# Performance work log

Measured on AMD Instinct MI355X. Metric: run time of the kernel, lower is better.

The kernel has to match this reference:

```python
import jax, jax.numpy as jnp
import numpy as np

M1, M2 = 32, 32  # max_modes1, max_modes2
C_IN, C_OUT = 64, 64


def _neg_k(a):
    # torch.roll(torch.flip(a, dims=[-2,-1]), shifts=(1,1), dims=[-2,-1])
    return jnp.roll(jnp.flip(a, axis=(-2, -1)), shift=(1, 1), axis=(-2, -1))


def compl_mul2d(x1, x2):
    x1n = _neg_k(x1)
    x2n = _neg_k(x2)
    e = lambda a, b: jnp.einsum('bixy,ioxy->boxy', a, b)
    return 0.5 * (e(x1, x2) - e(x1n, x2n) + e(x1, x2n) + e(x1n, x2))


def setup_inputs() -> dict:
    key = jax.random.key(0)
    k1, k2, k3 = jax.random.split(key, 3)
    scale = 1.0 / (C_IN * C_OUT)
    return {
        "x": jax.random.normal(k1, (16, C_IN, 256, 256), dtype=jnp.float32),
        "weights1_re": scale * jax.random.uniform(k2, (C_IN, C_OUT, M1, M2), dtype=jnp.float32),
        "weights1_im": scale * jax.random.uniform(k3, (C_IN, C_OUT, M1, M2), dtype=jnp.float32),
        "error_estimate": 1,  # must be >= 1: smaller modes would break the einsum vs full weights
    }


def reference(x, weights1_re, weights1_im, error_estimate):
    B, Ci, H, W = x.shape
    modes1 = min(M1, max(1, int(M1 * error_estimate)))
    modes2 = min(M2, max(1, int(M2 * error_estimate)))
    weights1 = jax.lax.complex(weights1_re, weights1_im)  # complex64

    # spectral branch (computed exactly as in the original; note the original
    # module never uses out_ft in its return value)
    x_ft = jnp.fft.rfftn(x, axes=(2, 3))  # [B, Ci, H, W//2+1] complex64
    block = compl_mul2d(x_ft[:, :, :modes1, :modes2], weights1)
    out_ft = jnp.zeros((B, C_OUT, H, W // 2 + 1), dtype=jnp.complex64)
    out_ft = out_ft.at[:, :, :modes1, :modes2].set(block)

    # idht(x) with dim=None: fftn over ALL axes, (real+imag)/numel
    X = jnp.fft.fftn(x, axes=(0, 1, 2, 3))
    out = (X.real + X.imag) / x.size
    return out.astype(jnp.float32)
```

## Files before the change

kernel.cpp:

```cpp
#include <hip/hip_runtime.h>


#define NB 16
#define NC 64
#define NH 256
#define NW 256
#define WP 132
#define CSTRIDE (NH*WP)
#define BSTRIDE (NC*NH*WP)
#define LSTRIDE (NH*WP)

__device__ __forceinline__ float2 cadd(float2 a, float2 b){ return make_float2(a.x+b.x, a.y+b.y); }
__device__ __forceinline__ float2 csub(float2 a, float2 b){ return make_float2(a.x-b.x, a.y-b.y); }
__device__ __forceinline__ float2 cmul(float2 a, float2 b){ return make_float2(a.x*b.x - a.y*b.y, a.x*b.y + a.y*b.x); }

__device__ __forceinline__ float2 twd(float frac){
  float sn, cs;
  __sincosf(-6.28318530717958647692f * frac, &sn, &cs);
  return make_float2(cs, sn);
}

__device__ __forceinline__ void dft4(float2&a,float2&b,float2&c,float2&d){
  float2 t0=cadd(a,c), t1=csub(a,c), t2=cadd(b,d), t3=csub(b,d);
  float2 t3i = make_float2(t3.y, -t3.x);
  a=cadd(t0,t2); c=csub(t0,t2); b=cadd(t1,t3i); d=csub(t1,t3i);
}

__device__ __forceinline__ void fft8(float2 v[8]){
  float2 e0=v[0],e1=v[2],e2=v[4],e3=v[6];
  float2 o0=v[1],o1=v[3],o2=v[5],o3=v[7];
  dft4(e0,e1,e2,e3); dft4(o0,o1,o2,o3);
  const float s=0.70710678118654752440f;
  float2 w1o=make_float2(s*(o1.x+o1.y), s*(o1.y-o1.x));
  float2 w2o=make_float2(o2.y, -o2.x);
  float2 w3o=make_float2(s*(o3.y-o3.x), -s*(o3.x+o3.y));
  v[0]=cadd(e0,o0); v[4]=csub(e0,o0);
  v[1]=cadd(e1,w1o); v[5]=csub(e1,w1o);
  v[2]=cadd(e2,w2o); v[6]=csub(e2,w2o);
  v[3]=cadd(e3,w3o); v[7]=csub(e3,w3o);
}

__device__ __forceinline__ void fft16(float2 v[16]){
  float2 e[8], o[8];
#pragma unroll
  for(int i=0;i<8;i++){ e[i]=v[2*i]; o[i]=v[2*i+1]; }
  fft8(e); fft8(o);
  const float c1=0.92387953251128675613f, s1=0.38268343236508977173f, s=0.70710678118654752440f;
  const float wr[8] = {1.f,  c1,  s,  s1, 0.f, -s1, -s, -c1};
  const float wi[8] = {0.f, -s1, -s, -c1, -1.f, -c1, -s, -s1};
#pragma unroll
  for(int k=0;k<8;k++){
    float2 wo = make_float2(wr[k]*o[k].x - wi[k]*o[k].y, wr[k]*o[k].y + wi[k]*o[k].x);
    v[k]=cadd(e[k],wo); v[k+8]=csub(e[k],wo);
  }
}

__global__ __launch_bounds__(256) void k1_fftW(const float* __restrict__ x, float2* __restrict__ S){
  __shared__ float2 lds[16][16][17];
  const int j    = threadIdx.x & 15;
  const int line = threadIdx.x >> 4;
  const int gline = blockIdx.x * 16 + line;
  const float* px = x + (size_t)gline * NW;
  float2 v[16];
#pragma unroll
  for(int n1=0;n1<16;n1++) v[n1] = make_float2(px[16*n1 + j], 0.f);
  fft16(v);
#pragma unroll
  for(int k1=0;k1<16;k1++){
    v[k1] = cmul(v[k1], twd((float)(j*k1) * (1.0f/256.0f)));
    lds[line][k1][j] = v[k1];
  }
  __syncthreads();
  float2 u[16];
#pragma unroll
  for(int n2=0;n2<16;n2++) u[n2] = lds[line][j][n2];
  fft16(u);
  float2* ps = S + (size_t)gline * WP;
#pragma unroll
  for(int k2=0;k2<8;k2++) ps[j + 16*k2] = u[k2];
  if(j==0) ps[128] = u[8];
}

__global__ __launch_bounds__(256) void k2_fftH(float2* __restrict__ S){
  __shared__ float2 lds[16][16][17];
  const int kwo  = threadIdx.x & 15;
  const int j    = threadIdx.x >> 4;
  const int tile = blockIdx.x % 9;
  const int slice= blockIdx.x / 9;
  const int kw   = tile*16 + kwo;
  const bool act = (kw <= 128);
  float2* base = S + (size_t)slice * NH * WP + kw;
  float2 v[16];
#pragma unroll
  for(int n1=0;n1<16;n1++) v[n1] = act ? base[(16*n1 + j) * WP] : make_float2(0.f,0.f);
  fft16(v);
#pragma unroll
  for(int k1=0;k1<16;k1++){
    v[k1] = cmul(v[k1], twd((float)(j*k1) * (1.0f/256.0f)));
    lds[kwo][k1][j] = v[k1];
  }
  __syncthreads();
  float2 u[16];
#pragma unroll
  for(int n2=0;n2<16;n2++) u[n2] = lds[kwo][j][n2];
  fft16(u);
  if(act){
#pragma unroll
    for(int k2=0;k2<16;k2++) base[(j + 16*k2) * WP] = u[k2];
  }
}

__global__ __launch_bounds__(256) void k3_fused(const float2* __restrict__ S, float* __restrict__ out){
  __shared__ float2 A[1024][9];
  const int t    = threadIdx.x;
  const int h    = blockIdx.x & 255;
  const int tile = blockIdx.x >> 8;
  const int kw0  = tile * 8;
  const float2* Sbase = S + (size_t)h * WP + kw0;

#pragma unroll
  for(int r=0;r<16;r++){
    int f    = t + 256*r;
    int line = f >> 2;
    int part = f & 3;
    float4 val;
    if(kw0 + part*2 + 1 < WP){
      val = *(const float4*)(Sbase + (size_t)line * LSTRIDE + part*2);
    } else {
      val = make_float4(0.f,0.f,0.f,0.f);
    }
    A[line][part*2]     = make_float2(val.x, val.y);
    A[line][part*2 + 1] = make_float2(val.z, val.w);
  }
  __syncthreads();

#pragma unroll
  for(int q=0;q<4;q++){
    int item = t + 256*q;
    int kwo = item & 7, n2 = (item>>3) & 7, b = item >> 6;
    float2 v[8];
#pragma unroll
    for(int n1=0;n1<8;n1++) v[n1] = A[b*64 + 8*n1 + n2][kwo];
    fft8(v);
#pragma unroll
    for(int k1=0;k1<8;k1++) A[b*64 + 8*k1 + n2][kwo] = cmul(v[k1], twd((float)(n2*k1) * (1.0f/64.0f)));
  }
  __syncthreads();

  {
    float2 u[4][8];
#pragma unroll
    for(int q=0;q<4;q++){
      int item = t + 256*q;
      int kwo = item & 7, k1 = (item>>3) & 7, b = item >> 6;
#pragma unroll
      for(int n2=0;n2<8;n2++) u[q][n2] = A[b*64 + 8*k1 + n2][kwo];
      fft8(u[q]);
    }
    __syncthreads();
#pragma unroll
    for(int q=0;q<4;q++){
      int item = t + 256*q;
      int kwo = item & 7, k1 = (item>>3) & 7, b = item >> 6;
#pragma unroll
      for(int k2=0;k2<8;k2++) A[b*64 + (k1 + 8*k2)][kwo] = u[q][k2];
    }
  }
  __syncthreads();

  const float inv = 1.0f / 67108864.0f;
  const int h2 = (NH - h) & 255;
#pragma unroll
  for(int q=0;q<2;q++){
    int item = t + 256*q;
    int kwo = item & 7, kc = item >> 3;
    float2 v[16];
#pragma unroll
    for(int b=0;b<16;b++) v[b] = A[b*64 + kc][kwo];
    fft16(v);
    const int kw = kw0 + kwo;
    if(kw <= 128){
      const int kc2 = (NC - kc) & 63;
#pragma unroll
      for(int kb=0;kb<16;kb++){
        float2 z = v[kb];
        out[(((size_t)kb*NC + kc)*NH + h)*NW + kw] = (z.x + z.y) * inv;
        if(kw >= 1 && kw <= 127){
          const int kb2 = (16 - kb) & 15;
          out[(((size_t)kb2*NC + kc2)*NH + h2)*NW + (NW - kw)] = (z.x - z.y) * inv;
        }
      }
    }
  }
}

extern "C" void kernel_launch(void* const* d_in, const int* in_sizes, int n_in,
                              void* d_out, int out_size, void* d_ws, size_t ws_size,
                              hipStream_t stream) {
  const float* x = (const float*)d_in[0];
  float* out = (float*)d_out;
  float2* S  = (float2*)d_ws;

  k1_fftW<<<NB*NC*NH/16, 256, 0, stream>>>(x, S);
  k2_fftH<<<NB*NC*9,     256, 0, stream>>>(S);
  k3_fused<<<17*256,     256, 0, stream>>>(S, out);
}
```

Measured before the change: 908.3 us.

## Stage k1 input via float4 LDS loads and widen k3 tiles with swizzled LDS

k1 now loads each block's 16 input rows into shared memory with coalesced float4 reads before the radix-16 passes, instead of strided scalar global reads. k3 processes 16 frequency columns per block with 1024 threads and stores its tile in an XOR-swizzled shared-memory layout, cutting the block count from 17*256 to 9*256 and making the staging stores 16-byte wide. The intent is better global coalescing and fewer LDS bank conflicts. The cost is 128 KB of LDS per k3 block, which limits occupancy to about one block per CU, plus an extra barrier in k1.

```diff
diff --git a/kernel.cpp b/kernel.cpp
--- a/kernel.cpp
+++ b/kernel.cpp
@@ -6,8 +6,6 @@
 #define NH 256
 #define NW 256
 #define WP 132
-#define CSTRIDE (NH*WP)
-#define BSTRIDE (NC*NH*WP)
 #define LSTRIDE (NH*WP)
 
 __device__ __forceinline__ float2 cadd(float2 a, float2 b){ return make_float2(a.x+b.x, a.y+b.y); }
@@ -56,33 +54,47 @@
 }
 
 __global__ __launch_bounds__(256) void k1_fftW(const float* __restrict__ x, float2* __restrict__ S){
-  __shared__ float2 lds[16][16][17];
-  const int j    = threadIdx.x & 15;
-  const int line = threadIdx.x >> 4;
-  const int gline = blockIdx.x * 16 + line;
-  const float* px = x + (size_t)gline * NW;
+  __shared__ __align__(16) float smem[16*273*2];
+  float2* lds2 = (float2*)smem;
+  const int t    = threadIdx.x;
+  const int j    = t & 15;
+  const int line = t >> 4;
+  const size_t gbase = (size_t)blockIdx.x * 16;
+
+  const float4* xv = (const float4*)x;
+#pragma unroll
+  for(int r=0;r<4;r++){
+    int f  = r*256 + t;
+    int ln = f >> 6, pos = f & 63;
+    float4 val = xv[(gbase + ln) * 64 + pos];
+    *(float4*)(&smem[ln*264 + pos*4]) = val;
+  }
+  __syncthreads();
+
   float2 v[16];
 #pragma unroll
-  for(int n1=0;n1<16;n1++) v[n1] = make_float2(px[16*n1 + j], 0.f);
+  for(int n1=0;n1<16;n1++) v[n1] = make_float2(smem[line*264 + 16*n1 + j], 0.f);
+  __syncthreads();
+
   fft16(v);
 #pragma unroll
   for(int k1=0;k1<16;k1++){
     v[k1] = cmul(v[k1], twd((float)(j*k1) * (1.0f/256.0f)));
-    lds[line][k1][j] = v[k1];
+    lds2[line*273 + k1*17 + j] = v[k1];
   }
   __syncthreads();
   float2 u[16];
 #pragma unroll
-  for(int n2=0;n2<16;n2++) u[n2] = lds[line][j][n2];
+  for(int n2=0;n2<16;n2++) u[n2] = lds2[line*273 + j*17 + n2];
   fft16(u);
-  float2* ps = S + (size_t)gline * WP;
+  float2* ps = S + (gbase + line) * WP;
 #pragma unroll
   for(int k2=0;k2<8;k2++) ps[j + 16*k2] = u[k2];
   if(j==0) ps[128] = u[8];
 }
 
 __global__ __launch_bounds__(256) void k2_fftH(float2* __restrict__ S){
-  __shared__ float2 lds[16][16][17];
+  __shared__ float2 lds[16*273];
   const int kwo  = threadIdx.x & 15;
   const int j    = threadIdx.x >> 4;
   const int tile = blockIdx.x % 9;
@@ -97,12 +109,12 @@
 #pragma unroll
   for(int k1=0;k1<16;k1++){
     v[k1] = cmul(v[k1], twd((float)(j*k1) * (1.0f/256.0f)));
-    lds[kwo][k1][j] = v[k1];
+    lds[kwo*273 + k1*17 + j] = v[k1];
   }
   __syncthreads();
   float2 u[16];
 #pragma unroll
-  for(int n2=0;n2<16;n2++) u[n2] = lds[kwo][j][n2];
+  for(int n2=0;n2<16;n2++) u[n2] = lds[kwo*273 + j*17 + n2];
   fft16(u);
   if(act){
 #pragma unroll
@@ -110,73 +122,71 @@
   }
 }
 
-__global__ __launch_bounds__(256) void k3_fused(const float2* __restrict__ S, float* __restrict__ out){
-  __shared__ float2 A[1024][9];
+#define AIX(row,kwo) (((row)<<4) + ((kwo) ^ (((row)&7)<<1)))
+__global__ __launch_bounds__(1024) void k3_fused(const float2* __restrict__ S, float* __restrict__ out){
+  __shared__ __align__(16) float2 A[1024*16];
   const int t    = threadIdx.x;
   const int h    = blockIdx.x & 255;
   const int tile = blockIdx.x >> 8;
-  const int kw0  = tile * 8;
+  const int kw0  = tile * 16;
   const float2* Sbase = S + (size_t)h * WP + kw0;
 
 #pragma unroll
-  for(int r=0;r<16;r++){
-    int f    = t + 256*r;
-    int line = f >> 2;
-    int part = f & 3;
+  for(int r=0;r<8;r++){
+    int f    = t + 1024*r;
+    int line = f >> 3;
+    int part = f & 7;
     float4 val;
     if(kw0 + part*2 + 1 < WP){
       val = *(const float4*)(Sbase + (size_t)line * LSTRIDE + part*2);
     } else {
       val = make_float4(0.f,0.f,0.f,0.f);
     }
-    A[line][part*2]     = make_float2(val.x, val.y);
-    A[line][part*2 + 1] = make_float2(val.z, val.w);
-  }
-  __syncthreads();
-
-#pragma unroll
-  for(int q=0;q<4;q++){
-    int item = t + 256*q;
-    int kwo = item & 7, n2 = (item>>3) & 7, b = item >> 6;
+    *(float4*)(&A[AIX(line, part*2)]) = val;
+  }
+  __syncthreads();
+
+#pragma unroll
+  for(int q=0;q<2;q++){
+    int item = t + 1024*q;
+    int kwo = item & 15, n2 = (item>>4) & 7, b = item >> 7;
     float2 v[8];
 #pragma unroll
-    for(int n1=0;n1<8;n1++) v[n1] = A[b*64 + 8*n1 + n2][kwo];
+    for(int n1=0;n1<8;n1++) v[n1] = A[AIX(b*64 + 8*n1 + n2, kwo)];
     fft8(v);
 #pragma unroll
-    for(int k1=0;k1<8;k1++) A[b*64 + 8*k1 + n2][kwo] = cmul(v[k1], twd((float)(n2*k1) * (1.0f/64.0f)));
+    for(int k1=0;k1<8;k1++) A[AIX(b*64 + 8*k1 + n2, kwo)] = cmul(v[k1], twd((float)(n2*k1) * (1.0f/64.0f)));
   }
   __syncthreads();
 
   {
-    float2 u[4][8];
-#pragma unroll
-    for(int q=0;q<4;q++){
-      int item = t + 256*q;
-      int kwo = item & 7, k1 = (item>>3) & 7, b = item >> 6;
-#pragma unroll
-      for(int n2=0;n2<8;n2++) u[q][n2] = A[b*64 + 8*k1 + n2][kwo];
+    float2 u[2][8];
+#pragma unroll
+    for(int q=0;q<2;q++){
+      int item = t + 1024*q;
+      int kwo = item & 15, k1 = (item>>4) & 7, b = item >> 7;
+#pragma unroll
+      for(int n2=0;n2<8;n2++) u[q][n2] = A[AIX(b*64 + 8*k1 + n2, kwo)];
       fft8(u[q]);
     }
     __syncthreads();
 #pragma unroll
-    for(int q=0;q<4;q++){
-      int item = t + 256*q;
-      int kwo = item & 7, k1 = (item>>3) & 7, b = item >> 6;
-#pragma unroll
-      for(int k2=0;k2<8;k2++) A[b*64 + (k1 + 8*k2)][kwo] = u[q][k2];
+    for(int q=0;q<2;q++){
+      int item = t + 1024*q;
+      int kwo = item & 15, k1 = (item>>4) & 7, b = item >> 7;
+#pragma unroll
+      for(int k2=0;k2<8;k2++) A[AIX(b*64 + (k1 + 8*k2), kwo)] = u[q][k2];
     }
   }
   __syncthreads();
 
   const float inv = 1.0f / 67108864.0f;
   const int h2 = (NH - h) & 255;
-#pragma unroll
-  for(int q=0;q<2;q++){
-    int item = t + 256*q;
-    int kwo = item & 7, kc = item >> 3;
+  {
+    int kwo = t & 15, kc = t >> 4;
     float2 v[16];
 #pragma unroll
-    for(int b=0;b<16;b++) v[b] = A[b*64 + kc][kwo];
+    for(int b=0;b<16;b++) v[b] = A[AIX(b*64 + kc, kwo)];
     fft16(v);
     const int kw = kw0 + kwo;
     if(kw <= 128){
@@ -201,7 +211,7 @@
   float* out = (float*)d_out;
   float2* S  = (float2*)d_ws;
 
-  k1_fftW<<<NB*NC*NH/16, 256, 0, stream>>>(x, S);
-  k2_fftH<<<NB*NC*9,     256, 0, stream>>>(S);
-  k3_fused<<<17*256,     256, 0, stream>>>(S, out);
-}
+  k1_fftW<<<NB*NC*NH/16, 256,  0, stream>>>(x, S);
+  k2_fftH<<<NB*NC*9,     256,  0, stream>>>(S);
+  k3_fused<<<9*256,      1024, 0, stream>>>(S, out);
+}
```

Measured after the change: 810.5 us. 1.12x faster.
